# Performance work log

Hardware: AMD Instinct MI355X
Metric: run time of the kernel (lower is better)

Reference implementation:

```python
import jax, jax.numpy as jnp
import numpy as np

B, N, C = 2, 2048, 1024
H = 16
D = C // H  # 64
EPS = 1e-6


def rms_norm(x, w):
    # LlamaRMSNorm: fp32 variance over last dim
    xf = x.astype(jnp.float32)
    var = jnp.mean(xf * xf, axis=-1, keepdims=True)
    xf = xf * jax.lax.rsqrt(var + EPS)
    return (w * xf).astype(x.dtype)


def setup_inputs() -> dict:
    key = jax.random.key(0)
    ks = jax.random.split(key, 4)
    x = jax.random.normal(ks[0], (B, N, C), dtype=jnp.float32)
    mask = jax.random.randint(ks[1], (B, N), 0, 2, dtype=jnp.int32)
    qkv_w = jax.random.normal(ks[2], (3 * C, C), dtype=jnp.float32) * (1.0 / np.sqrt(C))
    qkv_b = jnp.zeros((3 * C,), dtype=jnp.float32)
    proj_w = jax.random.normal(ks[3], (C, C), dtype=jnp.float32) * (1.0 / np.sqrt(C))
    proj_b = jnp.zeros((C,), dtype=jnp.float32)
    qn_w = jnp.ones((D,), dtype=jnp.float32)
    kn_w = jnp.ones((D,), dtype=jnp.float32)
    return {"x": x, "mask": mask, "qkv_w": qkv_w, "qkv_b": qkv_b,
            "proj_w": proj_w, "proj_b": proj_b, "qn_w": qn_w, "kn_w": kn_w}


def reference(x, mask, qkv_w, qkv_b, proj_w, proj_b, qn_w, kn_w):
    dtype = x.dtype
    scale = D ** -0.5
    # qkv projection -> (3, B, H, N, D)
    qkv = (x @ qkv_w.T + qkv_b).reshape(B, N, 3, H, D).transpose(2, 0, 3, 1, 4)
    q, k, v = qkv[0], qkv[1], qkv[2]
    q = rms_norm(q, qn_w)
    k = rms_norm(k, kn_w)
    q = q * scale
    # scores in fp32, key-padding mask [B,1,1,N]
    attn = jnp.einsum('bhnd,bhmd->bhnm', q, k).astype(jnp.float32)
    key_mask = (mask != 0)[:, None, None, :]
    attn = jnp.where(key_mask, attn, jnp.float32(-1e9))
    attn = jax.nn.softmax(attn, axis=-1).astype(dtype)
    out = jnp.einsum('bhnm,bhmd->bhnd', attn, v)  # (B,H,N,D)
    out = out.transpose(0, 2, 1, 3).reshape(B, N, C)
    return out @ proj_w.T + proj_b
```

## Files before the change

kernel.cpp:

```cpp
#include <hip/hip_runtime.h>
#include <hip/hip_bf16.h>
#include <stdint.h>
#include <math.h>

namespace {

constexpr int kB = 2;
constexpr int kN = 2048;
constexpr int kC = 1024;
constexpr int kH = 16;
constexpr int kD = 64;
constexpr int kTok = kB * kN;
constexpr int k3C  = 3 * kC;
constexpr size_t kPS = (size_t)kTok * k3C;
constexpr size_t kXE = (size_t)kTok * kC;
constexpr size_t kWQ = (size_t)k3C * kC;
constexpr size_t kWP = (size_t)kC * kC;

using bhalf8 = __attribute__((ext_vector_type(8))) __bf16;
using f32x4  = __attribute__((ext_vector_type(4))) float;

__device__ inline unsigned short f2bf(float f) {
  __hip_bfloat16 h = __float2bfloat16(f);
  return *reinterpret_cast<unsigned short*>(&h);
}
__device__ inline float bf2f(unsigned short u) {
  __hip_bfloat16 h;
  *reinterpret_cast<unsigned short*>(&h) = u;
  return __bfloat162float(h);
}
__device__ inline void split2(float v, unsigned short& h, unsigned short& l) {
  const unsigned short hb = f2bf(v);
  h = hb;
  l = f2bf(v - bf2f(hb));
}

#if __has_builtin(__builtin_amdgcn_exp2f)
__device__ inline float fexp2(float x) { return __builtin_amdgcn_exp2f(x); }
#else
__device__ inline float fexp2(float x) { return __expf(x * 0.6931471805599453f); }
#endif

__device__ inline void glds16(const unsigned short* g, unsigned short* l) {
  __builtin_amdgcn_global_load_lds(
      (const __attribute__((address_space(1))) void*)g,
      (__attribute__((address_space(3))) void*)l, 16, 0, 0);
}

__device__ inline void split4(const float4 v, ushort4& hh, ushort4& ll) {
  split2(v.x, hh.x, ll.x); split2(v.y, hh.y, ll.y);
  split2(v.z, hh.z, ll.z); split2(v.w, hh.w, ll.w);
}

__global__ __launch_bounds__(256)
void prep_split(const float* __restrict__ x, const float* __restrict__ wq,
                unsigned short* __restrict__ xH, unsigned short* __restrict__ xL,
                unsigned short* __restrict__ wqH, unsigned short* __restrict__ wqL)
{
  constexpr int nX = (int)(kXE / 4);
  int i = blockIdx.x * 256 + threadIdx.x;
  const float* src;
  unsigned short *H, *L;
  if (i < nX) { src = x;  H = xH;  L = xL; }
  else        { i -= nX; src = wq; H = wqH; L = wqL; }
  const float4 v = ((const float4*)src)[i];
  ushort4 hh, ll;
  split4(v, hh, ll);
  ((ushort4*)H)[i] = hh;
  ((ushort4*)L)[i] = ll;
}

__global__ __launch_bounds__(256)
void vt_and_split(const unsigned short* __restrict__ H,
                  unsigned short* __restrict__ VTH,
                  const float* __restrict__ wp,
                  unsigned short* __restrict__ wpH,
                  unsigned short* __restrict__ wpL)
{
  if (blockIdx.x < 2048) {
    const int gw   = blockIdx.x * 4 + (threadIdx.x >> 6);
    const int lane = threadIdx.x & 63;
    const int bh   = gw >> 8;
    const int oct  = gw & 255;
    const int b = bh >> 4, h = bh & 15;
    const int tok0 = oct * 8;
    union { unsigned short u[8]; uint4 v; } ph;
    #pragma unroll
    for (int e = 0; e < 8; ++e) {
      const size_t g = (size_t)(b * kN + tok0 + e) * k3C + 2 * kC + h * kD + lane;
      ph.u[e] = H[g];
    }
    *(uint4*)(&VTH[((size_t)bh * kD + lane) * kN + tok0]) = ph.v;
  } else {
    const int i = (blockIdx.x - 2048) * 256 + threadIdx.x;
    const float4 v = ((const float4*)wp)[i];
    ushort4 hh, ll;
    split4(v, hh, ll);
    ((ushort4*)wpH)[i] = hh;
    ((ushort4*)wpL)[i] = ll;
  }
}

__global__ __launch_bounds__(512)
void gemm_qkv256(const unsigned short* __restrict__ AH,
                 const unsigned short* __restrict__ AL,
                 const unsigned short* __restrict__ WH,
                 const unsigned short* __restrict__ WL,
                 const float* __restrict__ bias,
                 unsigned short* __restrict__ OutH,
                 unsigned short* __restrict__ OutL,
                 const float* __restrict__ qn,
                 const float* __restrict__ kn)
{
  constexpr int BK = 32;
  constexpr int NT = kC / BK;

  __shared__ __align__(16) unsigned short sA[2][2][256 * 32];
  __shared__ __align__(16) unsigned short sB[2][2][256 * 32];

  const int tt   = threadIdx.x;
  const int wave = tt >> 6;
  const int lane = tt & 63;
  const int quad = lane >> 4;
  const int l16  = lane & 15;
  const int bm = blockIdx.x * 256;
  const int bn = blockIdx.y * 256;
  const int wm = (wave >> 2) * 128;
  const int wn = (wave & 3) * 64;

  int srow[2], scol[2];
  #pragma unroll
  for (int r = 0; r < 2; ++r) {
    const int u = r * 512 + tt;
    srow[r] = u >> 2;
    scol[r] = ((u & 3) ^ ((srow[r] >> 1) & 3)) * 8;
  }

  auto stageU = [&](int bf, int k0, int which) {
    const unsigned short* src = (which == 0) ? AH : (which == 1) ? WH
                              : (which == 2) ? WL : AL;
    const int base = (which == 0 || which == 3) ? bm : bn;
    unsigned short* dst = (which == 0) ? &sA[bf][0][0]
                        : (which == 3) ? &sA[bf][1][0]
                        : (which == 1) ? &sB[bf][0][0] : &sB[bf][1][0];
    #pragma unroll
    for (int r = 0; r < 2; ++r)
      glds16(&src[(size_t)(base + srow[r]) * kC + k0 + scol[r]],
             &dst[(r * 512 + tt) * 8]);
  };

  auto rdA = [&](int bf, int pl, int row) -> bhalf8 {
    return *(const bhalf8*)(&sA[bf][pl][row * 32 + ((quad ^ ((row >> 1) & 3)) * 8)]);
  };
  auto rdB = [&](int bf, int pl, int row) -> bhalf8 {
    return *(const bhalf8*)(&sB[bf][pl][row * 32 + ((quad ^ ((row >> 1) & 3)) * 8)]);
  };

  f32x4 acc[8][4] = {};
  bhalf8 ah[8], bh_[4], bl_[4];

  stageU(0, 0, 0); stageU(0, 0, 1); stageU(0, 0, 2); stageU(0, 0, 3);
  asm volatile("s_waitcnt vmcnt(4)" ::: "memory");
  __builtin_amdgcn_sched_barrier(0);
  asm volatile("s_barrier" ::: "memory");

  for (int t = 0; t < NT - 1; ++t) {
    const int buf  = t & 1;
    const int nbuf = buf ^ 1;
    const int nk0  = (t + 1) * BK;

    #pragma unroll
    for (int i = 0; i < 8; ++i) ah[i]  = rdA(buf, 0, wm + i * 16 + l16);
    #pragma unroll
    for (int j = 0; j < 4; ++j) bh_[j] = rdB(buf, 0, wn + j * 16 + l16);
    stageU(nbuf, nk0, 0);
    stageU(nbuf, nk0, 1);
    asm volatile("s_waitcnt vmcnt(6)" ::: "memory");
    __builtin_amdgcn_sched_barrier(0);
    asm volatile("s_barrier" ::: "memory");
    __builtin_amdgcn_s_setprio(1);
    #pragma unroll
    for (int i = 0; i < 8; ++i)
      #pragma unroll
      for (int j = 0; j < 4; ++j)
        acc[i][j] = __builtin_amdgcn_mfma_f32_16x16x32_bf16(ah[i], bh_[j], acc[i][j], 0, 0, 0);
    __builtin_amdgcn_s_setprio(0);

    #pragma unroll
    for (int j = 0; j < 4; ++j) bl_[j] = rdB(buf, 1, wn + j * 16 + l16);
    stageU(nbuf, nk0, 2);
    asm volatile("s_waitcnt vmcnt(6)" ::: "memory");
    __builtin_amdgcn_sched_barrier(0);
    asm volatile("s_barrier" ::: "memory");
    __builtin_amdgcn_s_setprio(1);
    #pragma unroll
    for (int i = 0; i < 8; ++i)
      #pragma unroll
      for (int j = 0; j < 4; ++j)
        acc[i][j] = __builtin_amdgcn_mfma_f32_16x16x32_bf16(ah[i], bl_[j], acc[i][j], 0, 0, 0);
    __builtin_amdgcn_s_setprio(0);

    stageU(nbuf, nk0, 3);
    asm volatile("s_waitcnt vmcnt(4)" ::: "memory");
    __builtin_amdgcn_sched_barrier(0);
    asm volatile("s_barrier" ::: "memory");
    __builtin_amdgcn_s_setprio(1);
    {
      bhalf8 al0[4];
      #pragma unroll
      for (int i = 0; i < 4; ++i) al0[i] = rdA(buf, 1, wm + i * 16 + l16);
      #pragma unroll
      for (int i = 0; i < 4; ++i)
        #pragma unroll
        for (int j = 0; j < 4; ++j)
          acc[i][j] = __builtin_amdgcn_mfma_f32_16x16x32_bf16(al0[i], bh_[j], acc[i][j], 0, 0, 0);
      bhalf8 al1[4];
      #pragma unroll
      for (int i = 0; i < 4; ++i) al1[i] = rdA(buf, 1, wm + (4 + i) * 16 + l16);
      #pragma unroll
      for (int i = 0; i < 4; ++i)
        #pragma unroll
        for (int j = 0; j < 4; ++j)
          acc[4 + i][j] = __builtin_amdgcn_mfma_f32_16x16x32_bf16(al1[i], bh_[j], acc[4 + i][j], 0, 0, 0);
    }
    __builtin_amdgcn_s_setprio(0);
    asm volatile("s_barrier" ::: "memory");
  }

  {
    const int buf = (NT - 1) & 1;
    #pragma unroll
    for (int i = 0; i < 8; ++i) ah[i]  = rdA(buf, 0, wm + i * 16 + l16);
    #pragma unroll
    for (int j = 0; j < 4; ++j) bh_[j] = rdB(buf, 0, wn + j * 16 + l16);
    __builtin_amdgcn_s_setprio(1);
    #pragma unroll
    for (int i = 0; i < 8; ++i)
      #pragma unroll
      for (int j = 0; j < 4; ++j)
        acc[i][j] = __builtin_amdgcn_mfma_f32_16x16x32_bf16(ah[i], bh_[j], acc[i][j], 0, 0, 0);
    __builtin_amdgcn_s_setprio(0);

    asm volatile("s_waitcnt vmcnt(2)" ::: "memory");
    __builtin_amdgcn_sched_barrier(0);
    asm volatile("s_barrier" ::: "memory");
    #pragma unroll
    for (int j = 0; j < 4; ++j) bl_[j] = rdB(buf, 1, wn + j * 16 + l16);
    __builtin_amdgcn_s_setprio(1);
    #pragma unroll
    for (int i = 0; i < 8; ++i)
      #pragma unroll
      for (int j = 0; j < 4; ++j)
        acc[i][j] = __builtin_amdgcn_mfma_f32_16x16x32_bf16(ah[i], bl_[j], acc[i][j], 0, 0, 0);
    __builtin_amdgcn_s_setprio(0);

    asm volatile("s_waitcnt vmcnt(0)" ::: "memory");
    __builtin_amdgcn_sched_barrier(0);
    asm volatile("s_barrier" ::: "memory");
    __builtin_amdgcn_s_setprio(1);
    {
      bhalf8 al0[4];
      #pragma unroll
      for (int i = 0; i < 4; ++i) al0[i] = rdA(buf, 1, wm + i * 16 + l16);
      #pragma unroll
      for (int i = 0; i < 4; ++i)
        #pragma unroll
        for (int j = 0; j < 4; ++j)
          acc[i][j] = __builtin_amdgcn_mfma_f32_16x16x32_bf16(al0[i], bh_[j], acc[i][j], 0, 0, 0);
      bhalf8 al1[4];
      #pragma unroll
      for (int i = 0; i < 4; ++i) al1[i] = rdA(buf, 1, wm + (4 + i) * 16 + l16);
      #pragma unroll
      for (int i = 0; i < 4; ++i)
        #pragma unroll
        for (int j = 0; j < 4; ++j)
          acc[4 + i][j] = __builtin_amdgcn_mfma_f32_16x16x32_bf16(al1[i], bh_[j], acc[4 + i][j], 0, 0, 0);
    }
    __builtin_amdgcn_s_setprio(0);
  }

  const int slice = bn >> 10;
  const bool writeL = (slice == 0);
  float bv[4], wv[4];
  #pragma unroll
  for (int j = 0; j < 4; ++j) {
    bv[j] = bias[bn + wn + j * 16 + l16];
    if (slice < 2) wv[j] = (slice ? kn : qn)[j * 16 + l16];
  }

  #pragma unroll
  for (int i = 0; i < 8; ++i) {
    float val[4][4];
    #pragma unroll
    for (int j = 0; j < 4; ++j)
      #pragma unroll
      for (int r = 0; r < 4; ++r)
        val[j][r] = acc[i][j][r] + bv[j];

    if (slice < 2) {
      #pragma unroll
      for (int r = 0; r < 4; ++r) {
        float ss = val[0][r] * val[0][r];
        #pragma unroll
        for (int j = 1; j < 4; ++j) ss += val[j][r] * val[j][r];
        #pragma unroll
        for (int d = 1; d < 16; d <<= 1) ss += __shfl_xor(ss, d, 64);
        float rinv = rsqrtf(ss * (1.0f / 64.0f) + 1e-6f);
        if (slice == 0) rinv *= 0.18033688011112042f;
        #pragma unroll
        for (int j = 0; j < 4; ++j) val[j][r] = wv[j] * (val[j][r] * rinv);
      }
    }

    #pragma unroll
    for (int j = 0; j < 4; ++j) {
      const int n = bn + wn + j * 16 + l16;
      #pragma unroll
      for (int r = 0; r < 4; ++r) {
        const int m = bm + wm + i * 16 + quad * 4 + r;
        unsigned short hh, ll;
        split2(val[j][r], hh, ll);
        OutH[(size_t)m * k3C + n] = hh;
        if (writeL) OutL[(size_t)m * k3C + n] = ll;
      }
    }
  }
}

__global__ __launch_bounds__(256)
void gemm_proj128(const unsigned short* __restrict__ AH,
                  const unsigned short* __restrict__ AL,
                  const unsigned short* __restrict__ WH,
                  const unsigned short* __restrict__ WL,
                  const float* __restrict__ bias,
                  float* __restrict__ Out)
{
  constexpr int BK = 32;
  constexpr int NT = kC / BK;

  __shared__ __align__(16) unsigned short sA[2][2][128 * 32];
  __shared__ __align__(16) unsigned short sB[2][2][128 * 32];

  const int tt   = threadIdx.x;
  const int wave = tt >> 6;
  const int lane = tt & 63;
  const int quad = lane >> 4;
  const int l16  = lane & 15;
  const int bm = blockIdx.x * 128;
  const int bn = blockIdx.y * 128;
  const int wm = (wave >> 1) * 64;
  const int wn = (wave & 1) * 64;

  int srow[2], scol[2];
  #pragma unroll
  for (int r = 0; r < 2; ++r) {
    const int c = r * 256 + tt;
    srow[r] = c >> 2;
    scol[r] = ((c & 3) ^ ((srow[r] >> 1) & 3)) * 8;
  }

  auto stageU = [&](int bf, int k0, int which) {
    const unsigned short* src = (which == 0) ? AH : (which == 1) ? WH
                              : (which == 2) ? WL : AL;
    const bool isA = (which == 0 || which == 3);
    const int base = isA ? bm : bn;
    const int ld   = isA ? k3C : kC;
    unsigned short* dst = (which == 0) ? &sA[bf][0][0]
                        : (which == 3) ? &sA[bf][1][0]
                        : (which == 1) ? &sB[bf][0][0] : &sB[bf][1][0];
    #pragma unroll
    for (int r = 0; r < 2; ++r)
      glds16(&src[(size_t)(base + srow[r]) * ld + k0 + scol[r]],
             &dst[(r * 256 + tt) * 8]);
  };

  auto rdA = [&](int bf, int pl, int row) -> bhalf8 {
    return *(const bhalf8*)(&sA[bf][pl][row * 32 + ((quad ^ ((row >> 1) & 3)) * 8)]);
  };
  auto rdB = [&](int bf, int pl, int row) -> bhalf8 {
    return *(const bhalf8*)(&sB[bf][pl][row * 32 + ((quad ^ ((row >> 1) & 3)) * 8)]);
  };

  f32x4 acc[4][4] = {};
  bhalf8 ah[4], bh_[4], bl_[4];

  stageU(0, 0, 0); stageU(0, 0, 1); stageU(0, 0, 2); stageU(0, 0, 3);
  asm volatile("s_waitcnt vmcnt(4)" ::: "memory");
  __builtin_amdgcn_sched_barrier(0);
  asm volatile("s_barrier" ::: "memory");

  for (int t = 0; t < NT - 1; ++t) {
    const int buf  = t & 1;
    const int nbuf = buf ^ 1;
    const int nk0  = (t + 1) * BK;

    #pragma unroll
    for (int i = 0; i < 4; ++i) ah[i]  = rdA(buf, 0, wm + i * 16 + l16);
    #pragma unroll
    for (int j = 0; j < 4; ++j) bh_[j] = rdB(buf, 0, wn + j * 16 + l16);
    stageU(nbuf, nk0, 0);
    stageU(nbuf, nk0, 1);
    asm volatile("s_waitcnt vmcnt(6)" ::: "memory");
    __builtin_amdgcn_sched_barrier(0);
    asm volatile("s_barrier" ::: "memory");
    __builtin_amdgcn_s_setprio(1);
    #pragma unroll
    for (int i = 0; i < 4; ++i)
      #pragma unroll
      for (int j = 0; j < 4; ++j)
        acc[i][j] = __builtin_amdgcn_mfma_f32_16x16x32_bf16(ah[i], bh_[j], acc[i][j], 0, 0, 0);
    __builtin_amdgcn_s_setprio(0);

    #pragma unroll
    for (int j = 0; j < 4; ++j) bl_[j] = rdB(buf, 1, wn + j * 16 + l16);
    stageU(nbuf, nk0, 2);
    asm volatile("s_waitcnt vmcnt(6)" ::: "memory");
    __builtin_amdgcn_sched_barrier(0);
    asm volatile("s_barrier" ::: "memory");
    __builtin_amdgcn_s_setprio(1);
    #pragma unroll
    for (int i = 0; i < 4; ++i)
      #pragma unroll
      for (int j = 0; j < 4; ++j)
        acc[i][j] = __builtin_amdgcn_mfma_f32_16x16x32_bf16(ah[i], bl_[j], acc[i][j], 0, 0, 0);
    __builtin_amdgcn_s_setprio(0);

    stageU(nbuf, nk0, 3);
    asm volatile("s_waitcnt vmcnt(4)" ::: "memory");
    __builtin_amdgcn_sched_barrier(0);
    asm volatile("s_barrier" ::: "memory");
    __builtin_amdgcn_s_setprio(1);
    {
      bhalf8 al0[4];
      #pragma unroll
      for (int i = 0; i < 4; ++i) al0[i] = rdA(buf, 1, wm + i * 16 + l16);
      #pragma unroll
      for (int i = 0; i < 4; ++i)
        #pragma unroll
        for (int j = 0; j < 4; ++j)
          acc[i][j] = __builtin_amdgcn_mfma_f32_16x16x32_bf16(al0[i], bh_[j], acc[i][j], 0, 0, 0);
    }
    __builtin_amdgcn_s_setprio(0);
    asm volatile("s_barrier" ::: "memory");
  }

  {
    const int buf = (NT - 1) & 1;
    #pragma unroll
    for (int i = 0; i < 4; ++i) ah[i]  = rdA(buf, 0, wm + i * 16 + l16);
    #pragma unroll
    for (int j = 0; j < 4; ++j) bh_[j] = rdB(buf, 0, wn + j * 16 + l16);
    __builtin_amdgcn_s_setprio(1);
    #pragma unroll
    for (int i = 0; i < 4; ++i)
      #pragma unroll
      for (int j = 0; j < 4; ++j)
        acc[i][j] = __builtin_amdgcn_mfma_f32_16x16x32_bf16(ah[i], bh_[j], acc[i][j], 0, 0, 0);
    __builtin_amdgcn_s_setprio(0);

    asm volatile("s_waitcnt vmcnt(2)" ::: "memory");
    __builtin_amdgcn_sched_barrier(0);
    asm volatile("s_barrier" ::: "memory");
    #pragma unroll
    for (int j = 0; j < 4; ++j) bl_[j] = rdB(buf, 1, wn + j * 16 + l16);
    __builtin_amdgcn_s_setprio(1);
    #pragma unroll
    for (int i = 0; i < 4; ++i)
      #pragma unroll
      for (int j = 0; j < 4; ++j)
        acc[i][j] = __builtin_amdgcn_mfma_f32_16x16x32_bf16(ah[i], bl_[j], acc[i][j], 0, 0, 0);
    __builtin_amdgcn_s_setprio(0);

    asm volatile("s_waitcnt vmcnt(0)" ::: "memory");
    __builtin_amdgcn_sched_barrier(0);
    asm volatile("s_barrier" ::: "memory");
    __builtin_amdgcn_s_setprio(1);
    {
      bhalf8 al0[4];
      #pragma unroll
      for (int i = 0; i < 4; ++i) al0[i] = rdA(buf, 1, wm + i * 16 + l16);
      #pragma unroll
      for (int i = 0; i < 4; ++i)
        #pragma unroll
        for (int j = 0; j < 4; ++j)
          acc[i][j] = __builtin_amdgcn_mfma_f32_16x16x32_bf16(al0[i], bh_[j], acc[i][j], 0, 0, 0);
    }
    __builtin_amdgcn_s_setprio(0);
  }

  float bv[4];
  #pragma unroll
  for (int j = 0; j < 4; ++j) bv[j] = bias[bn + wn + j * 16 + l16];

  #pragma unroll
  for (int i = 0; i < 4; ++i)
    #pragma unroll
    for (int j = 0; j < 4; ++j) {
      const int n = bn + wn + j * 16 + l16;
      #pragma unroll
      for (int r = 0; r < 4; ++r) {
        const int m = bm + wm + i * 16 + quad * 4 + r;
        Out[(size_t)m * kC + n] = acc[i][j][r] + bv[j];
      }
    }
}

__global__ __launch_bounds__(256)
void attn_kernel(unsigned short* __restrict__ H, unsigned short* __restrict__ L,
                 const unsigned short* __restrict__ VTH,
                 const int* __restrict__ mask)
{
  constexpr int P   = 72;
  constexpr int Ppt = 68;
  __shared__ __align__(16) unsigned short KtH[2][64 * P];
  __shared__ __align__(16) unsigned short VtH[2][64 * P];
  __shared__ __align__(16) unsigned short Pt[4][32 * Ppt];

  const int t    = threadIdx.x;
  const int wave = t >> 6;
  const int lane = t & 63;
  const int quad = lane >> 4;
  const int l16  = lane & 15;

  const int lin  = blockIdx.x;
  const int xcd  = lin & 7;
  const int slot = lin >> 3;
  const int bh   = xcd + 8 * (slot >> 4);
  const int qblk = slot & 15;
  const int b  = bh >> 4;
  const int h  = bh & 15;
  const int q0 = qblk * 128 + wave * 32;

  const int row0 = t >> 3,         col0 = (t & 7) * 8;
  const int row1 = (256 + t) >> 3, col1 = ((256 + t) & 7) * 8;

  bhalf8 qfh[2][2], qfl[2][2];
  #pragma unroll
  for (int g = 0; g < 2; ++g) {
    const size_t qrow = (size_t)(b * kN + q0 + g * 16 + l16) * k3C + h * kD;
    qfh[g][0] = *(const bhalf8*)(&H[qrow + quad * 8]);
    qfh[g][1] = *(const bhalf8*)(&H[qrow + 32 + quad * 8]);
    qfl[g][0] = *(const bhalf8*)(&L[qrow + quad * 8]);
    qfl[g][1] = *(const bhalf8*)(&L[qrow + 32 + quad * 8]);
  }

  f32x4 acc_o[2][4] = {};
  float lpart[2][4] = {};

  uint4 sk0, sk1, sv0, sv1;
  int mcur[4], mnext[4];

  auto pref = [&](int kt) {
    sk0 = *(const uint4*)(&H[(size_t)(b * kN + kt + row0) * k3C + kC + h * kD + col0]);
    sk1 = *(const uint4*)(&H[(size_t)(b * kN + kt + row1) * k3C + kC + h * kD + col1]);
    sv0 = *(const uint4*)(&VTH[((size_t)bh * kD + row0) * kN + kt + col0]);
    sv1 = *(const uint4*)(&VTH[((size_t)bh * kD + row1) * kN + kt + col1]);
  };
  auto store_tile = [&](int bf) {
    *(uint4*)(&KtH[bf][row0 * P + col0]) = sk0;
    *(uint4*)(&KtH[bf][row1 * P + col1]) = sk1;
    *(uint4*)(&VtH[bf][row0 * P + col0]) = sv0;
    *(uint4*)(&VtH[bf][row1 * P + col1]) = sv1;
  };
  auto loadM = [&](int kt, int* m) {
    #pragma unroll
    for (int nt = 0; nt < 4; ++nt) m[nt] = mask[b * kN + kt + nt * 16 + l16];
  };

  pref(0);
  loadM(0, mcur);
  #pragma unroll
  for (int nt = 0; nt < 4; ++nt) mnext[nt] = mcur[nt];
  store_tile(0);
  pref(64);
  __syncthreads();

  for (int i = 0; i < 32; ++i) {
    const int cur = i & 1;
    const int kt = i * 64;
    if (i < 31) loadM(kt + 64, mnext);

    #pragma unroll
    for (int nt = 0; nt < 4; ++nt) {
      const int kr = (nt * 16 + l16) * P + quad * 8;
      const bhalf8 kh0 = *(const bhalf8*)(&KtH[cur][kr]);
      const bhalf8 kh1 = *(const bhalf8*)(&KtH[cur][kr + 32]);
      const float flag = mcur[nt] ? 1.0f : 0.0f;
      #pragma unroll
      for (int g = 0; g < 2; ++g) {
        f32x4 s = {};
        s = __builtin_amdgcn_mfma_f32_16x16x32_bf16(qfh[g][0], kh0, s, 0, 0, 0);
        s = __builtin_amdgcn_mfma_f32_16x16x32_bf16(qfh[g][1], kh1, s, 0, 0, 0);
        s = __builtin_amdgcn_mfma_f32_16x16x32_bf16(qfl[g][0], kh0, s, 0, 0, 0);
        s = __builtin_amdgcn_mfma_f32_16x16x32_bf16(qfl[g][1], kh1, s, 0, 0, 0);
        #pragma unroll
        for (int r = 0; r < 4; ++r) {
          const float p = flag * fexp2(s[r]);
          lpart[g][r] += p;
          Pt[wave][(g * 16 + quad * 4 + r) * Ppt + nt * 16 + l16] = f2bf(p);
        }
      }
    }

    #pragma unroll
    for (int kk = 0; kk < 2; ++kk) {
      const bhalf8 pa0 = *(const bhalf8*)(&Pt[wave][l16 * Ppt + kk * 32 + quad * 8]);
      const bhalf8 pa1 = *(const bhalf8*)(&Pt[wave][(16 + l16) * Ppt + kk * 32 + quad * 8]);
      #pragma unroll
      for (int dt = 0; dt < 4; ++dt) {
        const bhalf8 vb = *(const bhalf8*)(&VtH[cur][(dt * 16 + l16) * P + kk * 32 + quad * 8]);
        acc_o[0][dt] = __builtin_amdgcn_mfma_f32_16x16x32_bf16(pa0, vb, acc_o[0][dt], 0, 0, 0);
        acc_o[1][dt] = __builtin_amdgcn_mfma_f32_16x16x32_bf16(pa1, vb, acc_o[1][dt], 0, 0, 0);
      }
    }

    if (i < 31) {
      store_tile(cur ^ 1);
      if (i < 30) pref(kt + 128);
      __syncthreads();
      #pragma unroll
      for (int nt = 0; nt < 4; ++nt) mcur[nt] = mnext[nt];
    }
  }

  #pragma unroll
  for (int g = 0; g < 2; ++g)
    #pragma unroll
    for (int r = 0; r < 4; ++r) {
      float s = lpart[g][r];
      #pragma unroll
      for (int d = 1; d < 16; d <<= 1) s += __shfl_xor(s, d, 64);
      lpart[g][r] = s;
    }
  #pragma unroll
  for (int g = 0; g < 2; ++g)
    #pragma unroll
    for (int dt = 0; dt < 4; ++dt)
      #pragma unroll
      for (int r = 0; r < 4; ++r) {
        const int qrow = q0 + g * 16 + quad * 4 + r;
        const float inv = 1.0f / fmaxf(lpart[g][r], 1.0e-30f);
        const size_t off = (size_t)(b * kN + qrow) * k3C + h * kD + dt * 16 + l16;
        unsigned short hh, ll;
        split2(acc_o[g][dt][r] * inv, hh, ll);
        H[off] = hh; L[off] = ll;
      }
}

}

extern "C" void kernel_launch(void* const* d_in, const int* in_sizes, int n_in,
                              void* d_out, int out_size, void* d_ws, size_t ws_size,
                              hipStream_t stream)
{
  const float* x      = (const float*)d_in[0];
  const int*   maskp  = (const int*)d_in[1];
  const float* qkv_w  = (const float*)d_in[2];
  const float* qkv_b  = (const float*)d_in[3];
  const float* proj_w = (const float*)d_in[4];
  const float* proj_b = (const float*)d_in[5];
  const float* qn_w   = (const float*)d_in[6];
  const float* kn_w   = (const float*)d_in[7];
  float* out = (float*)d_out;

  unsigned short* qH = (unsigned short*)d_ws;
  unsigned short* qL = qH + kPS;
  unsigned short* R1 = qL + kPS;
  unsigned short* R2 = R1 + 2 * kXE;
  unsigned short* xH = R1,  *xL = R1 + kXE;
  unsigned short* VTH = R1;
  unsigned short* wqH = R2, *wqL = R2 + kWQ;
  unsigned short* wpH = R2, *wpL = R2 + kWP;

  prep_split<<<(int)((kXE + kWQ) / 4 / 256), 256, 0, stream>>>(
      x, qkv_w, xH, xL, wqH, wqL);

  gemm_qkv256<<<dim3(kTok / 256, k3C / 256), 512, 0, stream>>>(
      xH, xL, wqH, wqL, qkv_b, qH, qL, qn_w, kn_w);

  vt_and_split<<<3072, 256, 0, stream>>>(qH, VTH, proj_w, wpH, wpL);

  attn_kernel<<<dim3(512), 256, 0, stream>>>(qH, qL, VTH, maskp);

  gemm_proj128<<<dim3(kTok / 128, kC / 128), 256, 0, stream>>>(
      qH, qL, wpH, wpL, proj_b, out);
}
```

Baseline: 282.1 us.

## Retile QKV GEMM to 256x192 blocks with 8x1 wave layout

Changes the QKV projection GEMM from 256x256 tiles with a 2x4 wave grid to 256x192 tiles where each of 8 waves owns 32 rows across all 192 columns. The grid grows from 16x12 to 16x16 blocks, likely to give more even occupancy across the GPU's compute units. Only 6 of the 8 waves stage the weight tile, so the vmcnt waits are adjusted per wave. Each wave now rereads B fragments from LDS for every A fragment group, which raises LDS traffic per MFMA in exchange for a better-balanced grid.

```diff
diff --git a/kernel.cpp b/kernel.cpp
--- a/kernel.cpp
+++ b/kernel.cpp
@@ -116,7 +116,7 @@
   constexpr int NT = kC / BK;
 
   __shared__ __align__(16) unsigned short sA[2][2][256 * 32];
-  __shared__ __align__(16) unsigned short sB[2][2][256 * 32];
+  __shared__ __align__(16) unsigned short sB[2][2][192 * 32];
 
   const int tt   = threadIdx.x;
   const int wave = tt >> 6;
@@ -124,9 +124,9 @@
   const int quad = lane >> 4;
   const int l16  = lane & 15;
   const int bm = blockIdx.x * 256;
-  const int bn = blockIdx.y * 256;
-  const int wm = (wave >> 2) * 128;
-  const int wn = (wave & 3) * 64;
+  const int bn = blockIdx.y * 192;
+  const int wm = wave * 32;
+  const bool wstg = (wave < 6);
 
   int srow[2], scol[2];
   #pragma unroll
@@ -135,18 +135,28 @@
     srow[r] = u >> 2;
     scol[r] = ((u & 3) ^ ((srow[r] >> 1) & 3)) * 8;
   }
-
-  auto stageU = [&](int bf, int k0, int which) {
-    const unsigned short* src = (which == 0) ? AH : (which == 1) ? WH
-                              : (which == 2) ? WL : AL;
-    const int base = (which == 0 || which == 3) ? bm : bn;
-    unsigned short* dst = (which == 0) ? &sA[bf][0][0]
-                        : (which == 3) ? &sA[bf][1][0]
-                        : (which == 1) ? &sB[bf][0][0] : &sB[bf][1][0];
+  int wrow[2], wcol[2];
+  #pragma unroll
+  for (int r = 0; r < 2; ++r) {
+    const int c = r * 384 + tt;
+    wrow[r] = c >> 2;
+    wcol[r] = ((c & 3) ^ ((wrow[r] >> 1) & 3)) * 8;
+  }
+
+  auto stageA = [&](int bf, int k0, int pl) {
+    const unsigned short* src = pl ? AL : AH;
     #pragma unroll
     for (int r = 0; r < 2; ++r)
-      glds16(&src[(size_t)(base + srow[r]) * kC + k0 + scol[r]],
-             &dst[(r * 512 + tt) * 8]);
+      glds16(&src[(size_t)(bm + srow[r]) * kC + k0 + scol[r]],
+             &sA[bf][pl][(r * 512 + tt) * 8]);
+  };
+  auto stageW = [&](int bf, int k0, int pl) {
+    if (!wstg) return;
+    const unsigned short* src = pl ? WL : WH;
+    #pragma unroll
+    for (int r = 0; r < 2; ++r)
+      glds16(&src[(size_t)(bn + wrow[r]) * kC + k0 + wcol[r]],
+             &sB[bf][pl][(r * 384 + tt) * 8]);
   };
 
   auto rdA = [&](int bf, int pl, int row) -> bhalf8 {
@@ -156,11 +166,15 @@
     return *(const bhalf8*)(&sB[bf][pl][row * 32 + ((quad ^ ((row >> 1) & 3)) * 8)]);
   };
 
-  f32x4 acc[8][4] = {};
-  bhalf8 ah[8], bh_[4], bl_[4];
-
-  stageU(0, 0, 0); stageU(0, 0, 1); stageU(0, 0, 2); stageU(0, 0, 3);
-  asm volatile("s_waitcnt vmcnt(4)" ::: "memory");
+  f32x4 acc[2][12] = {};
+  bhalf8 ah[2], al[2], b4[4];
+
+  stageA(0, 0, 0);
+  stageW(0, 0, 0);
+  stageW(0, 0, 1);
+  stageA(0, 0, 1);
+  if (wstg) { asm volatile("s_waitcnt vmcnt(4)" ::: "memory"); }
+  else      { asm volatile("s_waitcnt vmcnt(2)" ::: "memory"); }
   __builtin_amdgcn_sched_barrier(0);
   asm volatile("s_barrier" ::: "memory");
 
@@ -169,59 +183,60 @@
     const int nbuf = buf ^ 1;
     const int nk0  = (t + 1) * BK;
 
-    #pragma unroll
-    for (int i = 0; i < 8; ++i) ah[i]  = rdA(buf, 0, wm + i * 16 + l16);
-    #pragma unroll
-    for (int j = 0; j < 4; ++j) bh_[j] = rdB(buf, 0, wn + j * 16 + l16);
-    stageU(nbuf, nk0, 0);
-    stageU(nbuf, nk0, 1);
-    asm volatile("s_waitcnt vmcnt(6)" ::: "memory");
-    __builtin_amdgcn_sched_barrier(0);
-    asm volatile("s_barrier" ::: "memory");
-    __builtin_amdgcn_s_setprio(1);
-    #pragma unroll
-    for (int i = 0; i < 8; ++i)
-      #pragma unroll
-      for (int j = 0; j < 4; ++j)
-        acc[i][j] = __builtin_amdgcn_mfma_f32_16x16x32_bf16(ah[i], bh_[j], acc[i][j], 0, 0, 0);
-    __builtin_amdgcn_s_setprio(0);
-
-    #pragma unroll
-    for (int j = 0; j < 4; ++j) bl_[j] = rdB(buf, 1, wn + j * 16 + l16);
-    stageU(nbuf, nk0, 2);
-    asm volatile("s_waitcnt vmcnt(6)" ::: "memory");
-    __builtin_amdgcn_sched_barrier(0);
-    asm volatile("s_barrier" ::: "memory");
-    __builtin_amdgcn_s_setprio(1);
-    #pragma unroll
-    for (int i = 0; i < 8; ++i)
-      #pragma unroll
-      for (int j = 0; j < 4; ++j)
-        acc[i][j] = __builtin_amdgcn_mfma_f32_16x16x32_bf16(ah[i], bl_[j], acc[i][j], 0, 0, 0);
-    __builtin_amdgcn_s_setprio(0);
-
-    stageU(nbuf, nk0, 3);
-    asm volatile("s_waitcnt vmcnt(4)" ::: "memory");
-    __builtin_amdgcn_sched_barrier(0);
-    asm volatile("s_barrier" ::: "memory");
-    __builtin_amdgcn_s_setprio(1);
-    {
-      bhalf8 al0[4];
-      #pragma unroll
-      for (int i = 0; i < 4; ++i) al0[i] = rdA(buf, 1, wm + i * 16 + l16);
-      #pragma unroll
-      for (int i = 0; i < 4; ++i)
+    ah[0] = rdA(buf, 0, wm + l16);
+    ah[1] = rdA(buf, 0, wm + 16 + l16);
+    stageA(nbuf, nk0, 0);
+    stageW(nbuf, nk0, 0);
+    if (wstg) asm volatile("s_waitcnt vmcnt(6)" ::: "memory");
+    __builtin_amdgcn_sched_barrier(0);
+    asm volatile("s_barrier" ::: "memory");
+    __builtin_amdgcn_s_setprio(1);
+    #pragma unroll
+    for (int jj = 0; jj < 3; ++jj) {
+      #pragma unroll
+      for (int j = 0; j < 4; ++j) b4[j] = rdB(buf, 0, jj * 64 + j * 16 + l16);
+      #pragma unroll
+      for (int i = 0; i < 2; ++i)
         #pragma unroll
         for (int j = 0; j < 4; ++j)
-          acc[i][j] = __builtin_amdgcn_mfma_f32_16x16x32_bf16(al0[i], bh_[j], acc[i][j], 0, 0, 0);
-      bhalf8 al1[4];
-      #pragma unroll
-      for (int i = 0; i < 4; ++i) al1[i] = rdA(buf, 1, wm + (4 + i) * 16 + l16);
-      #pragma unroll
-      for (int i = 0; i < 4; ++i)
+          acc[i][jj * 4 + j] = __builtin_amdgcn_mfma_f32_16x16x32_bf16(ah[i], b4[j], acc[i][jj * 4 + j], 0, 0, 0);
+    }
+    __builtin_amdgcn_s_setprio(0);
+
+    stageW(nbuf, nk0, 1);
+    if (wstg) asm volatile("s_waitcnt vmcnt(6)" ::: "memory");
+    __builtin_amdgcn_sched_barrier(0);
+    asm volatile("s_barrier" ::: "memory");
+    __builtin_amdgcn_s_setprio(1);
+    #pragma unroll
+    for (int jj = 0; jj < 3; ++jj) {
+      #pragma unroll
+      for (int j = 0; j < 4; ++j) b4[j] = rdB(buf, 1, jj * 64 + j * 16 + l16);
+      #pragma unroll
+      for (int i = 0; i < 2; ++i)
         #pragma unroll
         for (int j = 0; j < 4; ++j)
-          acc[4 + i][j] = __builtin_amdgcn_mfma_f32_16x16x32_bf16(al1[i], bh_[j], acc[4 + i][j], 0, 0, 0);
+          acc[i][jj * 4 + j] = __builtin_amdgcn_mfma_f32_16x16x32_bf16(ah[i], b4[j], acc[i][jj * 4 + j], 0, 0, 0);
+    }
+    __builtin_amdgcn_s_setprio(0);
+
+    stageA(nbuf, nk0, 1);
+    if (wstg) { asm volatile("s_waitcnt vmcnt(4)" ::: "memory"); }
+    else      { asm volatile("s_waitcnt vmcnt(2)" ::: "memory"); }
+    __builtin_amdgcn_sched_barrier(0);
+    asm volatile("s_barrier" ::: "memory");
+    __builtin_amdgcn_s_setprio(1);
+    al[0] = rdA(buf, 1, wm + l16);
+    al[1] = rdA(buf, 1, wm + 16 + l16);
+    #pragma unroll
+    for (int jj = 0; jj < 3; ++jj) {
+      #pragma unroll
+      for (int j = 0; j < 4; ++j) b4[j] = rdB(buf, 0, jj * 64 + j * 16 + l16);
+      #pragma unroll
+      for (int i = 0; i < 2; ++i)
+        #pragma unroll
+        for (int j = 0; j < 4; ++j)
+          acc[i][jj * 4 + j] = __builtin_amdgcn_mfma_f32_16x16x32_bf16(al[i], b4[j], acc[i][jj * 4 + j], 0, 0, 0);
     }
     __builtin_amdgcn_s_setprio(0);
     asm volatile("s_barrier" ::: "memory");
@@ -229,99 +244,98 @@
 
   {
     const int buf = (NT - 1) & 1;
-    #pragma unroll
-    for (int i = 0; i < 8; ++i) ah[i]  = rdA(buf, 0, wm + i * 16 + l16);
-    #pragma unroll
-    for (int j = 0; j < 4; ++j) bh_[j] = rdB(buf, 0, wn + j * 16 + l16);
-    __builtin_amdgcn_s_setprio(1);
-    #pragma unroll
-    for (int i = 0; i < 8; ++i)
-      #pragma unroll
-      for (int j = 0; j < 4; ++j)
-        acc[i][j] = __builtin_amdgcn_mfma_f32_16x16x32_bf16(ah[i], bh_[j], acc[i][j], 0, 0, 0);
-    __builtin_amdgcn_s_setprio(0);
-
-    asm volatile("s_waitcnt vmcnt(2)" ::: "memory");
-    __builtin_amdgcn_sched_barrier(0);
-    asm volatile("s_barrier" ::: "memory");
-    #pragma unroll
-    for (int j = 0; j < 4; ++j) bl_[j] = rdB(buf, 1, wn + j * 16 + l16);
-    __builtin_amdgcn_s_setprio(1);
-    #pragma unroll
-    for (int i = 0; i < 8; ++i)
-      #pragma unroll
-      for (int j = 0; j < 4; ++j)
-        acc[i][j] = __builtin_amdgcn_mfma_f32_16x16x32_bf16(ah[i], bl_[j], acc[i][j], 0, 0, 0);
+    ah[0] = rdA(buf, 0, wm + l16);
+    ah[1] = rdA(buf, 0, wm + 16 + l16);
+    __builtin_amdgcn_s_setprio(1);
+    #pragma unroll
+    for (int jj = 0; jj < 3; ++jj) {
+      #pragma unroll
+      for (int j = 0; j < 4; ++j) b4[j] = rdB(buf, 0, jj * 64 + j * 16 + l16);
+      #pragma unroll
+      for (int i = 0; i < 2; ++i)
+        #pragma unroll
+        for (int j = 0; j < 4; ++j)
+          acc[i][jj * 4 + j] = __builtin_amdgcn_mfma_f32_16x16x32_bf16(ah[i], b4[j], acc[i][jj * 4 + j], 0, 0, 0);
+    }
+    __builtin_amdgcn_s_setprio(0);
+
+    if (wstg) asm volatile("s_waitcnt vmcnt(2)" ::: "memory");
+    __builtin_amdgcn_sched_barrier(0);
+    asm volatile("s_barrier" ::: "memory");
+    __builtin_amdgcn_s_setprio(1);
+    #pragma unroll
+    for (int jj = 0; jj < 3; ++jj) {
+      #pragma unroll
+      for (int j = 0; j < 4; ++j) b4[j] = rdB(buf, 1, jj * 64 + j * 16 + l16);
+      #pragma unroll
+      for (int i = 0; i < 2; ++i)
+        #pragma unroll
+        for (int j = 0; j < 4; ++j)
+          acc[i][jj * 4 + j] = __builtin_amdgcn_mfma_f32_16x16x32_bf16(ah[i], b4[j], acc[i][jj * 4 + j], 0, 0, 0);
+    }
     __builtin_amdgcn_s_setprio(0);
 
     asm volatile("s_waitcnt vmcnt(0)" ::: "memory");
     __builtin_amdgcn_sched_barrier(0);
     asm volatile("s_barrier" ::: "memory");
     __builtin_amdgcn_s_setprio(1);
-    {
-      bhalf8 al0[4];
-      #pragma unroll
-      for (int i = 0; i < 4; ++i) al0[i] = rdA(buf, 1, wm + i * 16 + l16);
-      #pragma unroll
-      for (int i = 0; i < 4; ++i)
+    al[0] = rdA(buf, 1, wm + l16);
+    al[1] = rdA(buf, 1, wm + 16 + l16);
+    #pragma unroll
+    for (int jj = 0; jj < 3; ++jj) {
+      #pragma unroll
+      for (int j = 0; j < 4; ++j) b4[j] = rdB(buf, 0, jj * 64 + j * 16 + l16);
+      #pragma unroll
+      for (int i = 0; i < 2; ++i)
         #pragma unroll
         for (int j = 0; j < 4; ++j)
-          acc[i][j] = __builtin_amdgcn_mfma_f32_16x16x32_bf16(al0[i], bh_[j], acc[i][j], 0, 0, 0);
-      bhalf8 al1[4];
-      #pragma unroll
-      for (int i = 0; i < 4; ++i) al1[i] = rdA(buf, 1, wm + (4 + i) * 16 + l16);
-      #pragma unroll
-      for (int i = 0; i < 4; ++i)
-        #pragma unroll
-        for (int j = 0; j < 4; ++j)
-          acc[4 + i][j] = __builtin_amdgcn_mfma_f32_16x16x32_bf16(al1[i], bh_[j], acc[4 + i][j], 0, 0, 0);
-    }
-    __builtin_amdgcn_s_setprio(0);
-  }
-
-  const int slice = bn >> 10;
-  const bool writeL = (slice == 0);
-  float bv[4], wv[4];
-  #pragma unroll
-  for (int j = 0; j < 4; ++j) {
-    bv[j] = bias[bn + wn + j * 16 + l16];
-    if (slice < 2) wv[j] = (slice ? kn : qn)[j * 16 + l16];
-  }
-
-  #pragma unroll
-  for (int i = 0; i < 8; ++i) {
-    float val[4][4];
-    #pragma unroll
-    for (int j = 0; j < 4; ++j)
-      #pragma unroll
-      for (int r = 0; r < 4; ++r)
-        val[j][r] = acc[i][j][r] + bv[j];
-
-    if (slice < 2) {
-      #pragma unroll
-      for (int r = 0; r < 4; ++r) {
-        float ss = val[0][r] * val[0][r];
-        #pragma unroll
-        for (int j = 1; j < 4; ++j) ss += val[j][r] * val[j][r];
-        #pragma unroll
-        for (int d = 1; d < 16; d <<= 1) ss += __shfl_xor(ss, d, 64);
-        float rinv = rsqrtf(ss * (1.0f / 64.0f) + 1e-6f);
-        if (slice == 0) rinv *= 0.18033688011112042f;
-        #pragma unroll
-        for (int j = 0; j < 4; ++j) val[j][r] = wv[j] * (val[j][r] * rinv);
+          acc[i][jj * 4 + j] = __builtin_amdgcn_mfma_f32_16x16x32_bf16(al[i], b4[j], acc[i][jj * 4 + j], 0, 0, 0);
+    }
+    __builtin_amdgcn_s_setprio(0);
+  }
+
+  #pragma unroll
+  for (int i = 0; i < 2; ++i) {
+    #pragma unroll
+    for (int jj = 0; jj < 3; ++jj) {
+      const int n0 = bn + jj * 64;
+      const int slice = n0 >> 10;
+      const bool writeL = (slice == 0);
+      float val[4][4], wv[4];
+      #pragma unroll
+      for (int u = 0; u < 4; ++u) {
+        const float bv = bias[n0 + u * 16 + l16];
+        #pragma unroll
+        for (int r = 0; r < 4; ++r) val[u][r] = acc[i][jj * 4 + u][r] + bv;
+        if (slice < 2) wv[u] = (slice ? kn : qn)[u * 16 + l16];
       }
-    }
-
-    #pragma unroll
-    for (int j = 0; j < 4; ++j) {
-      const int n = bn + wn + j * 16 + l16;
-      #pragma unroll
-      for (int r = 0; r < 4; ++r) {
-        const int m = bm + wm + i * 16 + quad * 4 + r;
-        unsigned short hh, ll;
-        split2(val[j][r], hh, ll);
-        OutH[(size_t)m * k3C + n] = hh;
-        if (writeL) OutL[(size_t)m * k3C + n] = ll;
+
+      if (slice < 2) {
+        #pragma unroll
+        for (int r = 0; r < 4; ++r) {
+          float ss = val[0][r] * val[0][r];
+          #pragma unroll
+          for (int u = 1; u < 4; ++u) ss += val[u][r] * val[u][r];
+          #pragma unroll
+          for (int d = 1; d < 16; d <<= 1) ss += __shfl_xor(ss, d, 64);
+          float rinv = rsqrtf(ss * (1.0f / 64.0f) + 1e-6f);
+          if (slice == 0) rinv *= 0.18033688011112042f;
+          #pragma unroll
+          for (int u = 0; u < 4; ++u) val[u][r] = wv[u] * (val[u][r] * rinv);
+        }
+      }
+
+      #pragma unroll
+      for (int u = 0; u < 4; ++u) {
+        const int n = n0 + u * 16 + l16;
+        #pragma unroll
+        for (int r = 0; r < 4; ++r) {
+          const int m = bm + wm + i * 16 + quad * 4 + r;
+          unsigned short hh, ll;
+          split2(val[u][r], hh, ll);
+          OutH[(size_t)m * k3C + n] = hh;
+          if (writeL) OutL[(size_t)m * k3C + n] = ll;
+        }
       }
     }
   }
@@ -675,7 +689,7 @@
   prep_split<<<(int)((kXE + kWQ) / 4 / 256), 256, 0, stream>>>(
       x, qkv_w, xH, xL, wqH, wqL);
 
-  gemm_qkv256<<<dim3(kTok / 256, k3C / 256), 512, 0, stream>>>(
+  gemm_qkv256<<<dim3(kTok / 256, k3C / 192), 512, 0, stream>>>(
       xH, xL, wqH, wqL, qkv_b, qH, qL, qn_w, kn_w);
 
   vt_and_split<<<3072, 256, 0, stream>>>(qH, VTH, proj_w, wpH, wpL);
```

New measurement: 278.0 us (median of 2 runs). Within noise of the previous version (-1.5%).
